# Optimization experiments

Hardware: AMD Instinct MI355X
Metric: run time of the kernel (lower is better)

Reference implementation:

```python
import jax, jax.numpy as jnp
import numpy as np

N, E, IN_DIM, HID, HEADS, LAYERS, NUM_STORES = 50000, 800000, 64, 128, 16, 3, 50
DH = HID // HEADS  # per-head dim = 8
EPS = 1e-5


def setup_inputs() -> dict:
    key = jax.random.key(0)
    ks = iter(jax.random.split(key, 40))
    def nrm(shape, scale):
        return jax.random.normal(next(ks), shape, dtype=jnp.float32) * scale
    inp = {}
    inp['x'] = jax.random.normal(next(ks), (N, IN_DIM), dtype=jnp.float32)
    inp['edge_index'] = jax.random.randint(next(ks), (2, E), 0, N, dtype=jnp.int32)
    inp['edge_weight'] = jax.random.uniform(next(ks), (E, 1), dtype=jnp.float32)
    inp['store_mask'] = jax.random.randint(next(ks), (N,), 0, NUM_STORES, dtype=jnp.int32)
    # input_proj: Linear + GELU + LayerNorm
    inp['in_W'] = nrm((IN_DIM, HID), IN_DIM ** -0.5)
    inp['in_b'] = jnp.zeros((HID,), jnp.float32)
    inp['in_g'] = jnp.ones((HID,), jnp.float32)
    inp['in_beta'] = jnp.zeros((HID,), jnp.float32)
    # 3 stacked GATv2 layers (stacked leading dim = layer)
    s = HID ** -0.5
    inp['gat_Wl'] = nrm((LAYERS, HID, HID), s)
    inp['gat_bl'] = jnp.zeros((LAYERS, HID), jnp.float32)
    inp['gat_Wr'] = nrm((LAYERS, HID, HID), s)
    inp['gat_br'] = jnp.zeros((LAYERS, HID), jnp.float32)
    inp['gat_We'] = nrm((LAYERS, 1, HID), 1.0)
    inp['gat_att'] = nrm((LAYERS, HEADS, DH), DH ** -0.5)
    inp['gat_bias'] = jnp.zeros((LAYERS, HID), jnp.float32)
    inp['blk_g'] = jnp.ones((LAYERS, HID), jnp.float32)
    inp['blk_b'] = jnp.zeros((LAYERS, HID), jnp.float32)
    # per-store context gate + final norm
    inp['ctx_W'] = nrm((HID, HID), s)
    inp['ctx_b'] = jnp.zeros((HID,), jnp.float32)
    inp['fin_g'] = jnp.ones((HID,), jnp.float32)
    inp['fin_b'] = jnp.zeros((HID,), jnp.float32)
    return inp


def layernorm(x, g, b):
    mu = jnp.mean(x, axis=-1, keepdims=True)
    v = jnp.mean((x - mu) ** 2, axis=-1, keepdims=True)
    return (x - mu) * jax.lax.rsqrt(v + EPS) * g + b


def gatv2_layer(x, src, dst, ea, Wl, bl, Wr, br, We, att, bias):
    # x: [N, HID]; src/dst: [Et]; ea: [Et, 1]
    n = x.shape[0]
    xl = (x @ Wl + bl).reshape(n, HEADS, DH)   # source transform
    xr = (x @ Wr + br).reshape(n, HEADS, DH)   # target transform
    ee = (ea @ We).reshape(-1, HEADS, DH)      # edge-attr embedding
    e = jax.nn.leaky_relu(xl[src] + xr[dst] + ee, 0.2)  # [Et, H, D]
    logit = jnp.einsum('ehd,hd->eh', e, att)             # [Et, H]
    # segment softmax over incoming edges of each target node
    mx = jax.ops.segment_max(logit, dst, num_segments=n)
    p = jnp.exp(logit - mx[dst])
    Z = jax.ops.segment_sum(p, dst, num_segments=n)
    alpha = p / (Z[dst] + 1e-16)
    msg = alpha[:, :, None] * xl[src]                    # [Et, H, D]
    agg = jax.ops.segment_sum(msg, dst, num_segments=n)  # [N, H, D]
    return agg.reshape(n, HEADS * DH) + bias


def forward(x, edge_index, edge_weight, store_mask, in_W, in_b, in_g, in_beta,
            gat_Wl, gat_bl, gat_Wr, gat_br, gat_We, gat_att, gat_bias,
            blk_g, blk_b, ctx_W, ctx_b, fin_g, fin_b):
    n = x.shape[0]
    h = layernorm(jax.nn.gelu(x @ in_W + in_b, approximate=False), in_g, in_beta)
    src, dst = edge_index[0], edge_index[1]
    # PyG add_self_loops with fill_value='mean': per-target mean of incoming edge attrs
    deg = jax.ops.segment_sum(jnp.ones(src.shape, h.dtype), dst, num_segments=n)
    loop_attr = jax.ops.segment_sum(edge_weight, dst, num_segments=n) / jnp.maximum(deg, 1.0)[:, None]
    loops = jnp.arange(n, dtype=src.dtype)
    srcf = jnp.concatenate([src, loops])
    dstf = jnp.concatenate([dst, loops])
    eaf = jnp.concatenate([edge_weight, loop_attr], axis=0)
    for l in range(LAYERS):  # residual block: post-norm residual around conv
        m = gatv2_layer(h, srcf, dstf, eaf, gat_Wl[l], gat_bl[l], gat_Wr[l], gat_br[l],
                        gat_We[l], gat_att[l], gat_bias[l])
        h = layernorm(h + m, blk_g[l], blk_b[l])
    # per-store segmented mean -> sigmoid gate -> scatter back
    cnt = jax.ops.segment_sum(jnp.ones((n,), h.dtype), store_mask, num_segments=NUM_STORES)
    means = jax.ops.segment_sum(h, store_mask, num_segments=NUM_STORES) / jnp.maximum(cnt, 1.0)[:, None]
    gate = jax.nn.sigmoid(means @ ctx_W + ctx_b)
    h = h + (gate * means)[store_mask]
    return layernorm(h, fin_g, fin_b)


def reference(x, edge_index, edge_weight, store_mask, in_W, in_b, in_g, in_beta,
              gat_Wl, gat_bl, gat_Wr, gat_br, gat_We, gat_att, gat_bias,
              blk_g, blk_b, ctx_W, ctx_b, fin_g, fin_b):
    return forward(x, edge_index, edge_weight, store_mask, in_W, in_b, in_g, in_beta,
                   gat_Wl, gat_bl, gat_Wr, gat_br, gat_We, gat_att, gat_bias,
                   blk_g, blk_b, ctx_W, ctx_b, fin_g, fin_b)
```

## Files before the change

kernel.cpp:

```cpp
#include <hip/hip_runtime.h>
#include <math.h>

#define NN 50000
#define EE 800000
#define ET (EE + NN)
#define HID 128
#define NSTORE 50
#define NBL 196
#define CNT_B 3125
#define WCV_B 192
#define IWC_B 32
#define SCT_B2 1661
#define GEMB 391
#define SSB 512

typedef unsigned short ushort_t;
typedef unsigned long long u64;
typedef __attribute__((ext_vector_type(8))) short bf8;
typedef __attribute__((ext_vector_type(4))) float f4;
typedef __attribute__((ext_vector_type(2))) float f2;
typedef __attribute__((ext_vector_type(4))) unsigned int u4;

__device__ __forceinline__ ushort_t f2b(float f) {
    union { float f; unsigned int i; } v; v.f = f;
    unsigned int r = (v.i + 0x7fffu + ((v.i >> 16) & 1u)) >> 16;
    return (ushort_t)r;
}
__device__ __forceinline__ f2 b2f2v(unsigned int u) {
    union { unsigned int i; float f; } lo, hi;
    lo.i = u << 16; hi.i = u & 0xffff0000u;
    f2 r; r.x = lo.f; r.y = hi.f; return r;
}
__device__ __forceinline__ unsigned int pk2(float lo, float hi) {
    return (unsigned int)f2b(lo) | ((unsigned int)f2b(hi) << 16);
}
__device__ __forceinline__ f2 max2(f2 a, f2 b) {
#if __has_builtin(__builtin_elementwise_max)
    return __builtin_elementwise_max(a, b);
#else
    f2 r; r.x = fmaxf(a.x, b.x); r.y = fmaxf(a.y, b.y); return r;
#endif
}

__global__ __launch_bounds__(256) void k_build(const int* __restrict__ ei, const float* __restrict__ ew,
                                               const float* __restrict__ inW,
                                               const float* __restrict__ gWl, const float* __restrict__ gWr,
                                               ushort_t* __restrict__ inWt,
                                               ushort_t* __restrict__ Wlt, ushort_t* __restrict__ Wrt,
                                               u64* __restrict__ packed, int* __restrict__ rank) {
    int b = blockIdx.x, t = threadIdx.x;
    if (b < CNT_B) {
        int i = b * 256 + t;
        int dst = ei[EE + i];
        unsigned int wfix = __float2uint_rn(ew[i] * 16777216.0f);
        u64 old = atomicAdd(&packed[dst], (1ULL << 44) | (u64)wfix);
        rank[i] = (int)(old >> 44);
        return;
    }
    if (b < CNT_B + WCV_B) {
        int i = (b - CNT_B) * 256 + t;
        int l = i >> 14, r = i & 16383, nn2 = r >> 7, k = r & 127;
        Wlt[i] = f2b(gWl[(size_t)l * 16384 + k * 128 + nn2]);
        Wrt[i] = f2b(gWr[(size_t)l * 16384 + k * 128 + nn2]);
        return;
    }
    {
        int i = (b - CNT_B - WCV_B) * 256 + t;
        int c = i >> 6, k = i & 63;
        inWt[i] = f2b(inW[k * 128 + c]);
    }
}

__global__ __launch_bounds__(256) void k_inproj(const float* __restrict__ X,
                                                const ushort_t* __restrict__ Wt,
                                                const float* __restrict__ bias,
                                                const float* __restrict__ g,
                                                const float* __restrict__ be,
                                                ushort_t* __restrict__ hb) {
    const int K = 64;
    __shared__ float s1[2][128], s2[2][128];
    int lane = threadIdx.x & 63, w = threadIdx.x >> 6;
    int rw = w >> 1, cw = w & 1;
    int q = lane >> 4, l16 = lane & 15;
    int row0 = blockIdx.x * 128 + rw * 64;
    int col0 = cw * 64;
    bf8 z; for (int t = 0; t < 8; ++t) z[t] = 0;

    bf8 bfr[2][4];
#pragma unroll
    for (int kk = 0; kk < 2; ++kk)
#pragma unroll
        for (int j = 0; j < 4; ++j)
            bfr[kk][j] = *(const bf8*)(Wt + (size_t)(col0 + j * 16 + l16) * K + kk * 32 + q * 8);

    f4 acc[4][4];
#pragma unroll
    for (int i = 0; i < 4; ++i)
#pragma unroll
        for (int j = 0; j < 4; ++j) acc[i][j] = (f4)(0.f);

#pragma unroll
    for (int kk = 0; kk < 2; ++kk) {
        bf8 af[4];
#pragma unroll
        for (int i = 0; i < 4; ++i) {
            int r = row0 + i * 16 + l16;
            if (r < NN) {
                const float* xp = X + (size_t)r * K + kk * 32 + q * 8;
                f4 a = *(const f4*)xp;
                f4 c = *(const f4*)(xp + 4);
                u4 up; up.x = pk2(a.x, a.y); up.y = pk2(a.z, a.w);
                up.z = pk2(c.x, c.y); up.w = pk2(c.z, c.w);
                af[i] = *(bf8*)&up;
            } else af[i] = z;
        }
#pragma unroll
        for (int i = 0; i < 4; ++i)
#pragma unroll
            for (int j = 0; j < 4; ++j)
                acc[i][j] = __builtin_amdgcn_mfma_f32_16x16x32_bf16(af[i], bfr[kk][j], acc[i][j], 0, 0, 0);
    }
#pragma unroll
    for (int i = 0; i < 4; ++i) {
#pragma unroll
        for (int j = 0; j < 4; ++j) {
            float bv = bias[col0 + j * 16 + l16];
#pragma unroll
            for (int r = 0; r < 4; ++r) {
                float v = acc[i][j][r] + bv;
                v = 0.5f * v * (1.f + erff(v * 0.70710678118654752f));
                acc[i][j][r] = v;
            }
        }
    }
#pragma unroll
    for (int i = 0; i < 4; ++i) {
#pragma unroll
        for (int r = 0; r < 4; ++r) {
            float sm = acc[i][0][r] + acc[i][1][r] + acc[i][2][r] + acc[i][3][r];
            float sq = acc[i][0][r] * acc[i][0][r] + acc[i][1][r] * acc[i][1][r]
                     + acc[i][2][r] * acc[i][2][r] + acc[i][3][r] * acc[i][3][r];
#pragma unroll
            for (int k = 1; k < 16; k <<= 1) { sm += __shfl_xor(sm, k); sq += __shfl_xor(sq, k); }
            if (l16 == 0) {
                int rl = rw * 64 + i * 16 + q * 4 + r;
                s1[cw][rl] = sm; s2[cw][rl] = sq;
            }
        }
    }
    __syncthreads();
#pragma unroll
    for (int i = 0; i < 4; ++i) {
#pragma unroll
        for (int r = 0; r < 4; ++r) {
            int rl = rw * 64 + i * 16 + q * 4 + r;
            int gr = blockIdx.x * 128 + rl;
            if (gr >= NN) continue;
            float sm = s1[0][rl] + s1[1][rl];
            float sq = s2[0][rl] + s2[1][rl];
            float mu = sm * (1.f / 128.f);
            float var = sq * (1.f / 128.f) - mu * mu;
            float rinv = rsqrtf(var + 1e-5f);
#pragma unroll
            for (int j = 0; j < 4; ++j) {
                int gc = col0 + j * 16 + l16;
                float v = (acc[i][j][r] - mu) * rinv * g[gc] + be[gc];
                hb[(size_t)gr * HID + gc] = f2b(v);
            }
        }
    }
}

__global__ __launch_bounds__(256) void k_psum(const u64* __restrict__ packed, int* __restrict__ bsum) {
    int t = threadIdx.x, bidx = blockIdx.x;
    int i = bidx * 256 + t;
    int v = (i < NN) ? (int)(packed[i] >> 44) + 1 : 0;
#pragma unroll
    for (int d = 1; d < 64; d <<= 1) v += __shfl_xor(v, d);
    __shared__ int ws4[4];
    if ((t & 63) == 0) ws4[t >> 6] = v;
    __syncthreads();
    if (t == 0) bsum[bidx] = ws4[0] + ws4[1] + ws4[2] + ws4[3];
}

__global__ __launch_bounds__(256) void k_offs2(const u64* __restrict__ packed,
                                               const int* __restrict__ bsum, int* __restrict__ offs) {
    __shared__ int bws[4];
    __shared__ int wsum4[4];
    int t = threadIdx.x, bidx = blockIdx.x;
    int i = bidx * 256 + t;
    int v = (i < NN) ? (int)(packed[i] >> 44) + 1 : 0;
    int lane = t & 63, w = t >> 6;

    int bv = (t < bidx) ? bsum[t] : 0;
#pragma unroll
    for (int d = 1; d < 64; d <<= 1) bv += __shfl_xor(bv, d);
    if (lane == 0) bws[w] = bv;

    int sc = v;
#pragma unroll
    for (int d = 1; d < 64; d <<= 1) {
        int u = __shfl_up(sc, d);
        if (lane >= d) sc += u;
    }
    if (lane == 63) wsum4[w] = sc;
    __syncthreads();
    int base = bws[0] + bws[1] + bws[2] + bws[3];
    int wo = 0;
    for (int k = 0; k < w; ++k) wo += wsum4[k];
    if (i < NN) offs[i] = base + wo + sc - v;
    if (bidx == 0 && t == 0) offs[NN] = ET;
}

__global__ __launch_bounds__(512) void k_gemm2(const ushort_t* __restrict__ A,
                                               const ushort_t* __restrict__ Wt0,
                                               const ushort_t* __restrict__ Wt1,
                                               const float* __restrict__ b0,
                                               const float* __restrict__ b1,
                                               ushort_t* __restrict__ o0,
                                               ushort_t* __restrict__ o1, int n,
                                               const int* __restrict__ ei,
                                               const float* __restrict__ ew,
                                               const int* __restrict__ offs,
                                               const u64* __restrict__ packed,
                                               const int* __restrict__ rank,
                                               int2* __restrict__ csr) {
    int bid = blockIdx.x;
    if (bid >= GEMB) {
        int i = (bid - GEMB) * 512 + threadIdx.x;
        if (i < EE) {
            int src = ei[i], dst = ei[EE + i];
            int pos = offs[dst] + rank[i];
            int2 v; v.x = src << 8; v.y = __float_as_int(ew[i]);
            csr[pos] = v;
        } else if (i < ET) {
            int nd = i - EE;
            u64 p = packed[nd];
            int deg = (int)(p >> 44);
            float wsf = (float)(p & ((1ULL << 44) - 1)) * (1.0f / 16777216.0f);
            float la = wsf / fmaxf((float)deg, 1.0f);
            int pos = offs[nd + 1] - 1;
            int2 v; v.x = nd << 8; v.y = __float_as_int(la);
            csr[pos] = v;
        }
        return;
    }
    const int K = 128;
    __shared__ char As[128 * 256];
    int t = threadIdx.x;
    int row0 = bid * 128;
    bf8 z; for (int k = 0; k < 8; ++k) z[k] = 0;

    {
        int row = t >> 2, cq = t & 3;
        const ushort_t* srcp = A + (size_t)(row0 + row) * K + cq * 8;
        int swz = (row & 7) << 4;
        char* dst = As + row * 256;
        bool ok = (row0 + row) < n;
#pragma unroll
        for (int k = 0; k < 4; ++k) {
            bf8 v = ok ? *(const bf8*)(srcp + k * 32) : z;
            *(bf8*)(dst + ((k * 64 + cq * 16) ^ swz)) = v;
        }
    }
    __syncthreads();

    int w = t >> 6, lane = t & 63;
    int side = w >> 2, rw = (w >> 1) & 1, cw = w & 1;
    const ushort_t* Wt = side ? Wt1 : Wt0;
    const float* bias = side ? b1 : b0;
    ushort_t* outb = side ? o1 : o0;
    int q = lane >> 4, l16 = lane & 15;
    int col0 = cw * 64;

    f4 acc[4][4];
#pragma unroll
    for (int i = 0; i < 4; ++i)
#pragma unroll
        for (int j = 0; j < 4; ++j) acc[i][j] = (f4)(0.f);

#pragma unroll
    for (int kk = 0; kk < 4; ++kk) {
        bf8 bfk[4];
#pragma unroll
        for (int j = 0; j < 4; ++j)
            bfk[j] = *(const bf8*)(Wt + (size_t)(col0 + j * 16 + l16) * K + kk * 32 + q * 8);
        bf8 af[4];
#pragma unroll
        for (int i = 0; i < 4; ++i) {
            int r = rw * 64 + i * 16 + l16;
            af[i] = *(const bf8*)(As + r * 256 + ((kk * 64 + q * 16) ^ ((r & 7) << 4)));
        }
#pragma unroll
        for (int i = 0; i < 4; ++i)
#pragma unroll
            for (int j = 0; j < 4; ++j)
                acc[i][j] = __builtin_amdgcn_mfma_f32_16x16x32_bf16(af[i], bfk[j], acc[i][j], 0, 0, 0);
    }
#pragma unroll
    for (int i = 0; i < 4; ++i) {
        int gr0 = row0 + rw * 64 + i * 16 + q * 4;
#pragma unroll
        for (int j = 0; j < 4; ++j) {
            int gc = col0 + j * 16 + l16;
            float bv = bias[gc];
#pragma unroll
            for (int r = 0; r < 4; ++r) {
                int gr = gr0 + r;
                if (gr < n) outb[(size_t)gr * HID + gc] = f2b(acc[i][j][r] + bv);
            }
        }
    }
}

__global__ __launch_bounds__(256) void k_attn(const ushort_t* __restrict__ xl,
                                              const ushort_t* __restrict__ xr,
                                              ushort_t* __restrict__ hb,
                                              const int* __restrict__ offs,
                                              const int2* __restrict__ csr,
                                              const float* __restrict__ We,
                                              const float* __restrict__ att,
                                              const float* __restrict__ gbias,
                                              const float* __restrict__ g,
                                              const float* __restrict__ b) {
    int wid = (blockIdx.x * 256 + threadIdx.x) >> 6;
    int lane = threadIdx.x & 63;
    if (wid >= NN) return;
    int hd = lane & 15;
    int grp = lane >> 4;
    int dbase = hd * 8;
    int db2 = hd * 16;
    size_t base = (size_t)wid * HID;

    f2 xr2[4], at2[4], we2[4];
    {
        u4 uxr = *(const u4*)(xr + base + dbase);
        xr2[0] = b2f2v(uxr.x); xr2[1] = b2f2v(uxr.y);
        xr2[2] = b2f2v(uxr.z); xr2[3] = b2f2v(uxr.w);
        f4 a0 = *(const f4*)(att + dbase), a1 = *(const f4*)(att + dbase + 4);
        at2[0].x = a0.x; at2[0].y = a0.y; at2[1].x = a0.z; at2[1].y = a0.w;
        at2[2].x = a1.x; at2[2].y = a1.y; at2[3].x = a1.z; at2[3].y = a1.w;
        f4 w0 = *(const f4*)(We + dbase), w1 = *(const f4*)(We + dbase + 4);
        we2[0].x = w0.x; we2[0].y = w0.y; we2[1].x = w0.z; we2[1].y = w0.w;
        we2[2].x = w1.x; we2[2].y = w1.y; we2[3].x = w1.z; we2[3].y = w1.w;
    }
    int p0 = offs[wid], p1 = offs[wid + 1];
    float Z = 0.f;
    f2 acc2[4];
#pragma unroll
    for (int q = 0; q < 4; ++q) { acc2[q].x = 0.f; acc2[q].y = 0.f; }

#define LOADQ(UX, EA, VM)                                                      \
    {                                                                          \
        int ei_ = e + grp;                                                     \
        VM = (ei_ < p1);                                                       \
        int2 m2_ = csr[VM ? ei_ : (p1 - 1)];                                   \
        EA = __int_as_float(m2_.y);                                            \
        UX = *(const u4*)((const char*)xl + (unsigned)m2_.x + db2);            \
    }

#define COMPQ(UX, EA, VM)                                                      \
    {                                                                          \
        f2 x2_[4];                                                             \
        x2_[0] = b2f2v(UX.x); x2_[1] = b2f2v(UX.y);                            \
        x2_[2] = b2f2v(UX.z); x2_[3] = b2f2v(UX.w);                            \
        f2 lg2_; lg2_.x = 0.f; lg2_.y = 0.f;                                   \
        _Pragma("unroll")                                                      \
        for (int q_ = 0; q_ < 4; ++q_) {                                       \
            f2 t_ = (x2_[q_] + xr2[q_]) + EA * we2[q_];                        \
            t_ = max2(t_, t_ * 0.2f);                                          \
            lg2_ += at2[q_] * t_;                                              \
        }                                                                      \
        float w_ = VM ? __expf(lg2_.x + lg2_.y) : 0.f;                         \
        Z += w_;                                                               \
        _Pragma("unroll")                                                      \
        for (int q_ = 0; q_ < 4; ++q_) acc2[q_] += w_ * x2_[q_];               \
    }

    {
        u4 uxA, uxB; float eaA, eaB; bool vA, vB;
        int e = p0;
        LOADQ(uxA, eaA, vA)
        e += 4;
        while (e < p1) {
            LOADQ(uxB, eaB, vB)
            e += 4;
            COMPQ(uxA, eaA, vA)
            if (e >= p1) { COMPQ(uxB, eaB, vB) goto redux; }
            LOADQ(uxA, eaA, vA)
            e += 4;
            COMPQ(uxB, eaB, vB)
        }
        COMPQ(uxA, eaA, vA)
    }
redux:;
#undef LOADQ
#undef COMPQ

    Z += __shfl_xor(Z, 16); Z += __shfl_xor(Z, 32);
#pragma unroll
    for (int q = 0; q < 4; ++q) {
        acc2[q].x += __shfl_xor(acc2[q].x, 16);
        acc2[q].x += __shfl_xor(acc2[q].x, 32);
        acc2[q].y += __shfl_xor(acc2[q].y, 16);
        acc2[q].y += __shfl_xor(acc2[q].y, 32);
    }
    float inv = 1.f / (Z + 1e-16f);
    float acc[8] = {acc2[0].x, acc2[0].y, acc2[1].x, acc2[1].y,
                    acc2[2].x, acc2[2].y, acc2[3].x, acc2[3].y};

    u4 uh = *(const u4*)(hb + base + dbase);
    f2 hr0 = b2f2v(uh.x), hr1 = b2f2v(uh.y), hr2 = b2f2v(uh.z), hr3 = b2f2v(uh.w);
    float hres[8] = {hr0.x, hr0.y, hr1.x, hr1.y, hr2.x, hr2.y, hr3.x, hr3.y};
    f4 gb0 = *(const f4*)(gbias + dbase), gb1 = *(const f4*)(gbias + dbase + 4);
    float gb8[8] = {gb0.x, gb0.y, gb0.z, gb0.w, gb1.x, gb1.y, gb1.z, gb1.w};
    float o[8], sm = 0.f, sq = 0.f;
#pragma unroll
    for (int q = 0; q < 8; ++q) {
        o[q] = acc[q] * inv + gb8[q] + hres[q];
        sm += o[q]; sq += o[q] * o[q];
    }
#pragma unroll
    for (int k = 1; k < 16; k <<= 1) { sm += __shfl_xor(sm, k); sq += __shfl_xor(sq, k); }
    float mu = sm * (1.f / 128.f);
    float var = sq * (1.f / 128.f) - mu * mu;
    float rinv = rsqrtf(var + 1e-5f);
    f4 g0 = *(const f4*)(g + dbase), g1 = *(const f4*)(g + dbase + 4);
    float g8[8] = {g0.x, g0.y, g0.z, g0.w, g1.x, g1.y, g1.z, g1.w};
    f4 b0 = *(const f4*)(b + dbase), b1 = *(const f4*)(b + dbase + 4);
    float b8[8] = {b0.x, b0.y, b0.z, b0.w, b1.x, b1.y, b1.z, b1.w};
    float v8[8];
#pragma unroll
    for (int q = 0; q < 8; ++q) v8[q] = (o[q] - mu) * rinv * g8[q] + b8[q];
    if (grp == 0) {
        u4 hu;
        hu.x = pk2(v8[0], v8[1]); hu.y = pk2(v8[2], v8[3]);
        hu.z = pk2(v8[4], v8[5]); hu.w = pk2(v8[6], v8[7]);
        *(u4*)(hb + base + dbase) = hu;
    }
}

__global__ __launch_bounds__(256) void k_store_sum(const ushort_t* __restrict__ hb,
                                                   const int* __restrict__ mask,
                                                   float* __restrict__ psums,
                                                   int* __restrict__ pcnts) {
    __shared__ float ls[NSTORE * HID];
    __shared__ int lc[NSTORE];
    int t = threadIdx.x, bidx = blockIdx.x;
    for (int i = t; i < NSTORE * HID; i += 256) ls[i] = 0.f;
    if (t < NSTORE) lc[t] = 0;
    __syncthreads();
    int wid = bidx * 4 + (t >> 6);
    int lane = t & 63;
    int nw = SSB * 4;
    int d0 = lane * 2;
    for (int node = wid; node < NN; node += nw) {
        int s = mask[node];
        unsigned int hv = ((const unsigned int*)(hb + (size_t)node * HID))[lane];
        f2 v = b2f2v(hv);
        atomicAdd(&ls[s * HID + d0], v.x);
        atomicAdd(&ls[s * HID + d0 + 1], v.y);
        if (lane == 0) atomicAdd(&lc[s], 1);
    }
    __syncthreads();
    for (int i = t; i < NSTORE * HID; i += 256) psums[(size_t)bidx * (NSTORE * HID) + i] = ls[i];
    if (t < NSTORE) pcnts[bidx * NSTORE + t] = lc[t];
}

__global__ __launch_bounds__(256) void k_gate(const float* __restrict__ psums,
                                              const int* __restrict__ pcnts,
                                              const float* __restrict__ ctxW,
                                              const float* __restrict__ ctxb,
                                              float* __restrict__ gm) {
    __shared__ float h1[HID];
    __shared__ float mloc[HID];
    __shared__ int cw4[4];
    int s = blockIdx.x, t = threadIdx.x;
    int d = t & 127, half = t >> 7;
    float s0 = 0.f, s1 = 0.f, s2 = 0.f, s3 = 0.f;
    for (int b = half * 4; b < SSB; b += 8) {
        s0 += psums[(size_t)(b + 0) * (NSTORE * HID) + s * HID + d];
        s1 += psums[(size_t)(b + 1) * (NSTORE * HID) + s * HID + d];
        s2 += psums[(size_t)(b + 2) * (NSTORE * HID) + s * HID + d];
        s3 += psums[(size_t)(b + 3) * (NSTORE * HID) + s * HID + d];
    }
    float sum = (s0 + s1) + (s2 + s3);
    int c = pcnts[t * NSTORE + s] + pcnts[(t + 256) * NSTORE + s];
#pragma unroll
    for (int k = 1; k < 64; k <<= 1) c += __shfl_xor(c, k);
    if ((t & 63) == 0) cw4[t >> 6] = c;
    if (half) h1[d] = sum;
    __syncthreads();
    if (half == 0) {
        float tot = sum + h1[d];
        float cnt = fmaxf((float)(cw4[0] + cw4[1] + cw4[2] + cw4[3]), 1.f);
        mloc[d] = tot / cnt;
    }
    __syncthreads();
    if (half == 0) {
        float acc = ctxb[d];
        for (int j = 0; j < HID; ++j) acc += mloc[j] * ctxW[j * HID + d];
        float gate = 1.f / (1.f + __expf(-acc));
        gm[s * HID + d] = gate * mloc[d];
    }
}

__global__ __launch_bounds__(256) void k_final(const ushort_t* __restrict__ hb,
                                               const int* __restrict__ mask,
                                               const float* __restrict__ gm,
                                               const float* __restrict__ g,
                                               const float* __restrict__ b,
                                               float* __restrict__ out) {
    int wid = (blockIdx.x * 256 + threadIdx.x) >> 6;
    int lane = threadIdx.x & 63;
    if (wid >= NN) return;
    size_t base = (size_t)wid * HID;
    int s = mask[wid];
    int d0 = lane * 2, d1 = d0 + 1;
    unsigned int hv = ((const unsigned int*)(hb + base))[lane];
    f2 hvv = b2f2v(hv);
    float v0 = hvv.x + gm[s * HID + d0];
    float v1 = hvv.y + gm[s * HID + d1];
    float sm = v0 + v1, sq = v0 * v0 + v1 * v1;
#pragma unroll
    for (int k = 1; k < 64; k <<= 1) { sm += __shfl_xor(sm, k); sq += __shfl_xor(sq, k); }
    float mu = sm * (1.f / 128.f);
    float var = sq * (1.f / 128.f) - mu * mu;
    float r = rsqrtf(var + 1e-5f);
    out[base + d0] = (v0 - mu) * r * g[d0] + b[d0];
    out[base + d1] = (v1 - mu) * r * g[d1] + b[d1];
}

extern "C" void kernel_launch(void* const* d_in, const int* in_sizes, int n_in,
                              void* d_out, int out_size, void* d_ws, size_t ws_size,
                              hipStream_t stream) {
    const float* x      = (const float*)d_in[0];
    const int*   ei     = (const int*)d_in[1];
    const float* ew     = (const float*)d_in[2];
    const int*   smask  = (const int*)d_in[3];
    const float* inW    = (const float*)d_in[4];
    const float* inb    = (const float*)d_in[5];
    const float* ing    = (const float*)d_in[6];
    const float* inbeta = (const float*)d_in[7];
    const float* gWl    = (const float*)d_in[8];
    const float* gbl    = (const float*)d_in[9];
    const float* gWr    = (const float*)d_in[10];
    const float* gbr    = (const float*)d_in[11];
    const float* gWe    = (const float*)d_in[12];
    const float* gatt   = (const float*)d_in[13];
    const float* gbias  = (const float*)d_in[14];
    const float* blkg   = (const float*)d_in[15];
    const float* blkb   = (const float*)d_in[16];
    const float* ctxW   = (const float*)d_in[17];
    const float* ctxb   = (const float*)d_in[18];
    const float* fing   = (const float*)d_in[19];
    const float* finb   = (const float*)d_in[20];
    float* out = (float*)d_out;

    float* ws = (float*)d_ws;
    size_t o = 0;
    int2*     csr    = (int2*)(ws + o);     o += (size_t)ET * 2;
    float*    gm     = ws + o;              o += NSTORE * HID;
    int*      offs   = (int*)(ws + o);      o += 50004;
    int*      rank   = (int*)(ws + o);      o += EE;
    ushort_t* hb     = (ushort_t*)(ws + o); o += (size_t)NN * HID / 2;
    ushort_t* xlb    = (ushort_t*)(ws + o); o += (size_t)NN * HID / 2;
    ushort_t* xrb    = (ushort_t*)(ws + o); o += (size_t)NN * HID / 2;
    ushort_t* inWt   = (ushort_t*)(ws + o); o += 128 * 64 / 2;
    ushort_t* Wlt    = (ushort_t*)(ws + o); o += 3 * 128 * 128 / 2;
    ushort_t* Wrt    = (ushort_t*)(ws + o); o += 3 * 128 * 128 / 2;
    int*      bsum   = (int*)(ws + o);      o += 256;
    float*    psums  = ws + o;              o += (size_t)SSB * NSTORE * HID;
    int*      pcnts  = (int*)(ws + o);      o += SSB * NSTORE;
    if (o & 1) ++o;
    float*    zbase  = ws + o;
    u64*      packed = (u64*)(ws + o);      o += (size_t)NN * 2;
    size_t zbytes = (size_t)(NN * 2) * 4;

    hipMemsetAsync((void*)zbase, 0, zbytes, stream);

    const int WB = NN / 4;

    k_build<<<CNT_B + WCV_B + IWC_B, 256, 0, stream>>>(ei, ew, inW, gWl, gWr,
                                                       inWt, Wlt, Wrt, packed, rank);
    k_inproj<<<GEMB, 256, 0, stream>>>(x, inWt, inb, ing, inbeta, hb);
    k_psum<<<NBL, 256, 0, stream>>>(packed, bsum);
    k_offs2<<<NBL, 256, 0, stream>>>(packed, bsum, offs);

    for (int l = 0; l < 3; ++l) {
        int nb = GEMB + (l == 0 ? SCT_B2 : 0);
        k_gemm2<<<nb, 512, 0, stream>>>(hb, Wlt + (size_t)l * HID * HID, Wrt + (size_t)l * HID * HID,
                                        gbl + l * HID, gbr + l * HID, xlb, xrb, NN,
                                        ei, ew, offs, packed, rank, csr);
        k_attn<<<WB, 256, 0, stream>>>(xlb, xrb, hb, offs, csr,
                                       gWe + l * HID, gatt + l * HID, gbias + l * HID,
                                       blkg + l * HID, blkb + l * HID);
    }

    k_store_sum<<<SSB, 256, 0, stream>>>(hb, smask, psums, pcnts);
    k_gate<<<NSTORE, 256, 0, stream>>>(psums, pcnts, ctxW, ctxb, gm);
    k_final<<<WB, 256, 0, stream>>>(hb, smask, gm, fing, finb, out);
}
```

Before: 475.4 us.

## Pack degree/weight into 32-bit atomics and move CSR scatter into input projection

Degree counting now uses 32-bit atomics: the count sits in the top 8 bits and a coarser fixed-point weight sum in the low 24 bits, replacing 64-bit atomics and halving the zeroed buffer. The offset scan now runs before the input projection, so the CSR scatter blocks move out of the first layer GEMM and into the input-projection launch. Each attention launch is split into two half-node launches. Together these aim to cut atomic and memset traffic and shorten the first layer's critical path. The trade-offs are lower precision in the self-loop weight mean, an 8-bit degree field that would overflow above 255, and extra launch overhead from the split.

Measured after the change: 496.3 us. +4.4%, slower.

```diff
diff --git a/kernel.cpp b/kernel.cpp
--- a/kernel.cpp
+++ b/kernel.cpp
@@ -10,12 +10,13 @@
 #define CNT_B 3125
 #define WCV_B 192
 #define IWC_B 32
-#define SCT_B2 1661
+#define SCT_B 3321
 #define GEMB 391
 #define SSB 512
+#define WB2 6250
 
 typedef unsigned short ushort_t;
-typedef unsigned long long u64;
+typedef unsigned int u32;
 typedef __attribute__((ext_vector_type(8))) short bf8;
 typedef __attribute__((ext_vector_type(4))) float f4;
 typedef __attribute__((ext_vector_type(2))) float f2;
@@ -47,14 +48,14 @@
                                                const float* __restrict__ gWl, const float* __restrict__ gWr,
                                                ushort_t* __restrict__ inWt,
                                                ushort_t* __restrict__ Wlt, ushort_t* __restrict__ Wrt,
-                                               u64* __restrict__ packed, int* __restrict__ rank) {
+                                               u32* __restrict__ packed, int* __restrict__ rank) {
     int b = blockIdx.x, t = threadIdx.x;
     if (b < CNT_B) {
         int i = b * 256 + t;
         int dst = ei[EE + i];
-        unsigned int wfix = __float2uint_rn(ew[i] * 16777216.0f);
-        u64 old = atomicAdd(&packed[dst], (1ULL << 44) | (u64)wfix);
-        rank[i] = (int)(old >> 44);
+        unsigned int wfix = __float2uint_rn(ew[i] * 262144.0f);
+        unsigned int old = atomicAdd(&packed[dst], (1u << 24) | wfix);
+        rank[i] = (int)(old >> 24);
         return;
     }
     if (b < CNT_B + WCV_B) {
@@ -71,12 +72,78 @@
     }
 }
 
+__global__ __launch_bounds__(256) void k_psum(const u32* __restrict__ packed, int* __restrict__ bsum) {
+    int t = threadIdx.x, bidx = blockIdx.x;
+    int i = bidx * 256 + t;
+    int v = (i < NN) ? (int)(packed[i] >> 24) + 1 : 0;
+#pragma unroll
+    for (int d = 1; d < 64; d <<= 1) v += __shfl_xor(v, d);
+    __shared__ int ws4[4];
+    if ((t & 63) == 0) ws4[t >> 6] = v;
+    __syncthreads();
+    if (t == 0) bsum[bidx] = ws4[0] + ws4[1] + ws4[2] + ws4[3];
+}
+
+__global__ __launch_bounds__(256) void k_offs2(const u32* __restrict__ packed,
+                                               const int* __restrict__ bsum, int* __restrict__ offs) {
+    __shared__ int bws[4];
+    __shared__ int wsum4[4];
+    int t = threadIdx.x, bidx = blockIdx.x;
+    int i = bidx * 256 + t;
+    int v = (i < NN) ? (int)(packed[i] >> 24) + 1 : 0;
+    int lane = t & 63, w = t >> 6;
+
+    int bv = (t < bidx) ? bsum[t] : 0;
+#pragma unroll
+    for (int d = 1; d < 64; d <<= 1) bv += __shfl_xor(bv, d);
+    if (lane == 0) bws[w] = bv;
+
+    int sc = v;
+#pragma unroll
+    for (int d = 1; d < 64; d <<= 1) {
+        int u = __shfl_up(sc, d);
+        if (lane >= d) sc += u;
+    }
+    if (lane == 63) wsum4[w] = sc;
+    __syncthreads();
+    int base = bws[0] + bws[1] + bws[2] + bws[3];
+    int wo = 0;
+    for (int k = 0; k < w; ++k) wo += wsum4[k];
+    if (i < NN) offs[i] = base + wo + sc - v;
+    if (bidx == 0 && t == 0) offs[NN] = ET;
+}
+
 __global__ __launch_bounds__(256) void k_inproj(const float* __restrict__ X,
                                                 const ushort_t* __restrict__ Wt,
                                                 const float* __restrict__ bias,
                                                 const float* __restrict__ g,
                                                 const float* __restrict__ be,
-                                                ushort_t* __restrict__ hb) {
+                                                ushort_t* __restrict__ hb,
+                                                const int* __restrict__ ei,
+                                                const float* __restrict__ ew,
+                                                const int* __restrict__ offs,
+                                                const u32* __restrict__ packed,
+                                                const int* __restrict__ rank,
+                                                int2* __restrict__ csr) {
+    if (blockIdx.x >= GEMB) {
+        int i = (blockIdx.x - GEMB) * 256 + threadIdx.x;
+        if (i < EE) {
+            int src = ei[i], dst = ei[EE + i];
+            int pos = offs[dst] + rank[i];
+            int2 v; v.x = src << 8; v.y = __float_as_int(ew[i]);
+            csr[pos] = v;
+        } else if (i < ET) {
+            int nd = i - EE;
+            u32 p = packed[nd];
+            int deg = (int)(p >> 24);
+            float wsf = (float)(p & 0xFFFFFFu) * (1.0f / 262144.0f);
+            float la = wsf / fmaxf((float)deg, 1.0f);
+            int pos = offs[nd + 1] - 1;
+            int2 v; v.x = nd << 8; v.y = __float_as_int(la);
+            csr[pos] = v;
+        }
+        return;
+    }
     const int K = 64;
     __shared__ float s1[2][128], s2[2][128];
     int lane = threadIdx.x & 63, w = threadIdx.x >> 6;
@@ -171,80 +238,14 @@
     }
 }
 
-__global__ __launch_bounds__(256) void k_psum(const u64* __restrict__ packed, int* __restrict__ bsum) {
-    int t = threadIdx.x, bidx = blockIdx.x;
-    int i = bidx * 256 + t;
-    int v = (i < NN) ? (int)(packed[i] >> 44) + 1 : 0;
-#pragma unroll
-    for (int d = 1; d < 64; d <<= 1) v += __shfl_xor(v, d);
-    __shared__ int ws4[4];
-    if ((t & 63) == 0) ws4[t >> 6] = v;
-    __syncthreads();
-    if (t == 0) bsum[bidx] = ws4[0] + ws4[1] + ws4[2] + ws4[3];
-}
-
-__global__ __launch_bounds__(256) void k_offs2(const u64* __restrict__ packed,
-                                               const int* __restrict__ bsum, int* __restrict__ offs) {
-    __shared__ int bws[4];
-    __shared__ int wsum4[4];
-    int t = threadIdx.x, bidx = blockIdx.x;
-    int i = bidx * 256 + t;
-    int v = (i < NN) ? (int)(packed[i] >> 44) + 1 : 0;
-    int lane = t & 63, w = t >> 6;
-
-    int bv = (t < bidx) ? bsum[t] : 0;
-#pragma unroll
-    for (int d = 1; d < 64; d <<= 1) bv += __shfl_xor(bv, d);
-    if (lane == 0) bws[w] = bv;
-
-    int sc = v;
-#pragma unroll
-    for (int d = 1; d < 64; d <<= 1) {
-        int u = __shfl_up(sc, d);
-        if (lane >= d) sc += u;
-    }
-    if (lane == 63) wsum4[w] = sc;
-    __syncthreads();
-    int base = bws[0] + bws[1] + bws[2] + bws[3];
-    int wo = 0;
-    for (int k = 0; k < w; ++k) wo += wsum4[k];
-    if (i < NN) offs[i] = base + wo + sc - v;
-    if (bidx == 0 && t == 0) offs[NN] = ET;
-}
-
 __global__ __launch_bounds__(512) void k_gemm2(const ushort_t* __restrict__ A,
                                                const ushort_t* __restrict__ Wt0,
                                                const ushort_t* __restrict__ Wt1,
                                                const float* __restrict__ b0,
                                                const float* __restrict__ b1,
                                                ushort_t* __restrict__ o0,
-                                               ushort_t* __restrict__ o1, int n,
-                                               const int* __restrict__ ei,
-                                               const float* __restrict__ ew,
-                                               const int* __restrict__ offs,
-                                               const u64* __restrict__ packed,
-                                               const int* __restrict__ rank,
-                                               int2* __restrict__ csr) {
+                                               ushort_t* __restrict__ o1, int n) {
     int bid = blockIdx.x;
-    if (bid >= GEMB) {
-        int i = (bid - GEMB) * 512 + threadIdx.x;
-        if (i < EE) {
-            int src = ei[i], dst = ei[EE + i];
-            int pos = offs[dst] + rank[i];
-            int2 v; v.x = src << 8; v.y = __float_as_int(ew[i]);
-            csr[pos] = v;
-        } else if (i < ET) {
-            int nd = i - EE;
-            u64 p = packed[nd];
-            int deg = (int)(p >> 44);
-            float wsf = (float)(p & ((1ULL << 44) - 1)) * (1.0f / 16777216.0f);
-            float la = wsf / fmaxf((float)deg, 1.0f);
-            int pos = offs[nd + 1] - 1;
-            int2 v; v.x = nd << 8; v.y = __float_as_int(la);
-            csr[pos] = v;
-        }
-        return;
-    }
     const int K = 128;
     __shared__ char As[128 * 256];
     int t = threadIdx.x;
@@ -322,8 +323,9 @@
                                               const float* __restrict__ att,
                                               const float* __restrict__ gbias,
                                               const float* __restrict__ g,
-                                              const float* __restrict__ b) {
-    int wid = (blockIdx.x * 256 + threadIdx.x) >> 6;
+                                              const float* __restrict__ b,
+                                              int n0) {
+    int wid = n0 + ((blockIdx.x * 256 + threadIdx.x) >> 6);
     int lane = threadIdx.x & 63;
     if (wid >= NN) return;
     int hd = lane & 15;
@@ -572,29 +574,29 @@
     int*      bsum   = (int*)(ws + o);      o += 256;
     float*    psums  = ws + o;              o += (size_t)SSB * NSTORE * HID;
     int*      pcnts  = (int*)(ws + o);      o += SSB * NSTORE;
-    if (o & 1) ++o;
-    float*    zbase  = ws + o;
-    u64*      packed = (u64*)(ws + o);      o += (size_t)NN * 2;
-    size_t zbytes = (size_t)(NN * 2) * 4;
-
-    hipMemsetAsync((void*)zbase, 0, zbytes, stream);
+    u32*      packed = (u32*)(ws + o);      o += NN;
+    size_t zbytes = (size_t)NN * 4;
+
+    hipMemsetAsync((void*)packed, 0, zbytes, stream);
 
     const int WB = NN / 4;
 
     k_build<<<CNT_B + WCV_B + IWC_B, 256, 0, stream>>>(ei, ew, inW, gWl, gWr,
                                                        inWt, Wlt, Wrt, packed, rank);
-    k_inproj<<<GEMB, 256, 0, stream>>>(x, inWt, inb, ing, inbeta, hb);
     k_psum<<<NBL, 256, 0, stream>>>(packed, bsum);
     k_offs2<<<NBL, 256, 0, stream>>>(packed, bsum, offs);
+    k_inproj<<<GEMB + SCT_B, 256, 0, stream>>>(x, inWt, inb, ing, inbeta, hb,
+                                               ei, ew, offs, packed, rank, csr);
 
     for (int l = 0; l < 3; ++l) {
-        int nb = GEMB + (l == 0 ? SCT_B2 : 0);
-        k_gemm2<<<nb, 512, 0, stream>>>(hb, Wlt + (size_t)l * HID * HID, Wrt + (size_t)l * HID * HID,
-                                        gbl + l * HID, gbr + l * HID, xlb, xrb, NN,
-                                        ei, ew, offs, packed, rank, csr);
-        k_attn<<<WB, 256, 0, stream>>>(xlb, xrb, hb, offs, csr,
-                                       gWe + l * HID, gatt + l * HID, gbias + l * HID,
-                                       blkg + l * HID, blkb + l * HID);
+        k_gemm2<<<GEMB, 512, 0, stream>>>(hb, Wlt + (size_t)l * HID * HID, Wrt + (size_t)l * HID * HID,
+                                          gbl + l * HID, gbr + l * HID, xlb, xrb, NN);
+        k_attn<<<WB2, 256, 0, stream>>>(xlb, xrb, hb, offs, csr,
+                                        gWe + l * HID, gatt + l * HID, gbias + l * HID,
+                                        blkg + l * HID, blkb + l * HID, 0);
+        k_attn<<<WB2, 256, 0, stream>>>(xlb, xrb, hb, offs, csr,
+                                        gWe + l * HID, gatt + l * HID, gbias + l * HID,
+                                        blkg + l * HID, blkb + l * HID, 25000);
     }
 
     k_store_sum<<<SSB, 256, 0, stream>>>(hb, smask, psums, pcnts);
```
